# Optimization experiments

Hardware: AMD Instinct MI355X
Metric: run time of the kernel (lower is better)

## Reference

```python
import jax, jax.numpy as jnp
import numpy as np

CODEBOOK_SIZE = 1024
CODEWORD_SIZE = 256
BETA = 0.1
N_INIT = 1  # embedding ~ U(-1/n, 1/n)


def setup_inputs() -> dict:
    key = jax.random.key(0)
    kx, ke = jax.random.split(key)
    x = jax.random.normal(kx, (16, 4096, CODEWORD_SIZE), dtype=jnp.float32)
    embedding = jax.random.uniform(
        ke, (CODEBOOK_SIZE, CODEWORD_SIZE), dtype=jnp.float32,
        minval=-1.0 / N_INIT, maxval=1.0 / N_INIT)
    return {"x": x, "embedding": embedding}


def reference(x, embedding):
    dist = (jnp.sum(x * x, axis=2, keepdims=True)
            + jnp.sum(embedding * embedding, axis=1)
            - 2.0 * jnp.einsum('btd,kd->btk', x, embedding))
    indexes = jnp.argmin(dist, axis=2)              # [B,T] int
    values = jnp.take(embedding, indexes, axis=0)   # gather == one_hot @ embedding
    sg = jax.lax.stop_gradient
    loss1 = jnp.mean((sg(x) - values) ** 2)         # codebook loss
    loss2 = jnp.mean((x - sg(values)) ** 2)         # commitment loss
    loss = loss1 + BETA * loss2
    values_st = x + sg(values - x)                  # straight-through
    return values_st, indexes, loss
```

## Files before the change

kernel.cpp:

```cpp
#include <hip/hip_runtime.h>
#include <stdint.h>


#define BT    65536
#define D     256
#define KCB   1024
#define BM    256
#define BN    128
#define NTT   (KCB/BN)
#define BK    32

typedef float    f32x4 __attribute__((ext_vector_type(4)));
typedef _Float16 f16x8 __attribute__((ext_vector_type(8)));

#define GLOAD_LDS16(g, l) \
  __builtin_amdgcn_global_load_lds((const __attribute__((address_space(1))) void*)(g), \
                                   (__attribute__((address_space(3))) void*)(l), 16, 0, 0)

__global__ __launch_bounds__(256) void split_e_kernel(const float* __restrict__ E,
                                                      _Float16* __restrict__ Eh,
                                                      _Float16* __restrict__ El,
                                                      float* __restrict__ enorm,
                                                      float* __restrict__ out_loss) {
    if (blockIdx.x == 0 && threadIdx.x == 0) *out_loss = 0.f;
    const int r = blockIdx.x * 8 + (threadIdx.x >> 5);
    const size_t i0 = (size_t)r * D + (threadIdx.x & 31) * 8;
    float4 v0 = *(const float4*)(E + i0);
    float4 v1 = *(const float4*)(E + i0 + 4);
    float v[8] = {v0.x, v0.y, v0.z, v0.w, v1.x, v1.y, v1.z, v1.w};
    f16x8 h, l;
    float s = 0.f;
    #pragma unroll
    for (int j = 0; j < 8; ++j) {
        _Float16 hh = (_Float16)v[j];
        h[j] = hh;
        l[j] = (_Float16)(v[j] - (float)hh);
        s += v[j] * v[j];
    }
    *(f16x8*)(Eh + i0) = h;
    *(f16x8*)(El + i0) = l;
    #pragma unroll
    for (int off = 1; off < 32; off <<= 1) s += __shfl_xor(s, off, 64);
    if ((threadIdx.x & 31) == 0) enorm[r] = s;
}

__global__ __launch_bounds__(512, 2) void vq_mfma_kernel(
    const float* __restrict__ X,
    const _Float16* __restrict__ Eh, const _Float16* __restrict__ El,
    const float* __restrict__ enorm, const float* __restrict__ E,
    float* __restrict__ out_vals, float* __restrict__ out_idx,
    float* __restrict__ out_loss) {
    __shared__ __align__(16) float    Xs[64 * D];
    __shared__ __align__(16) _Float16 Bsh[2][BN * BK];
    __shared__ __align__(16) _Float16 Bsl[2][BN * BK];
    __shared__ float s_en[KCB];
    __shared__ float s_bd[BM];
    __shared__ int   s_bi[BM];
    __shared__ float s_red[8];

    const int tid  = threadIdx.x;
    const int w    = tid >> 6;
    const int lane = tid & 63;
    const int quad = lane >> 4;
    const int l16  = lane & 15;
    const int sxa  = l16 & 7;
    const int row0 = blockIdx.x * BM;

    const int sb_row = lane >> 2;
    const int sb_off = ((((lane & 3) - (lane >> 3)) & 3) << 3);
    const int kob = ((quad + ((l16 >> 1) & 3)) & 3) << 3;

    auto STAGE_B = [&](int buf, int col0, int kb) {
        const int gr = col0 + w * 16 + sb_row;
        const size_t gb = (size_t)gr * D + kb + sb_off;
        GLOAD_LDS16(Eh + gb, &Bsh[buf][w * 512]);
        GLOAD_LDS16(El + gb, &Bsl[buf][w * 512]);
    };

    s_en[tid]       = enorm[tid];
    s_en[tid + 512] = enorm[tid + 512];

    STAGE_B(0, 0, 0);

    f16x8 pah[2][8], pal[2][8];
    float xs = 0.f;
    for (int p = 0; p < 4; ++p) {
        #pragma unroll
        for (int rr = 0; rr < 8; ++rr) {
            const int sr = w * 8 + rr;
            const int gr = row0 + p * 64 + sr;
            GLOAD_LDS16(X + (size_t)gr * D + ((lane ^ rr) << 2), &Xs[sr * D]);
        }
        asm volatile("s_waitcnt vmcnt(0) lgkmcnt(0)" ::: "memory");
        __builtin_amdgcn_s_barrier();
        if ((w >> 1) == p) {
            const int srb = (w & 1) * 32;
            #pragma unroll
            for (int i = 0; i < 2; ++i) {
                const float* rp = &Xs[(srb + i * 16 + l16) * D];
                #pragma unroll
                for (int kc = 0; kc < 8; ++kc) {
                    const int c0 = kc * 8 + quad * 2;
                    const f32x4 v0 = *(const f32x4*)(rp + (((c0)     ^ sxa) << 2));
                    const f32x4 v1 = *(const f32x4*)(rp + (((c0 | 1) ^ sxa) << 2));
                    const float f[8] = {v0.x, v0.y, v0.z, v0.w, v1.x, v1.y, v1.z, v1.w};
                    #pragma unroll
                    for (int e = 0; e < 8; ++e) {
                        const _Float16 hh = (_Float16)f[e];
                        pah[i][kc][e] = hh;
                        pal[i][kc][e] = (_Float16)(f[e] - (float)hh);
                        xs += f[e] * f[e];
                    }
                }
            }
        }
        __builtin_amdgcn_s_barrier();
    }

    float rb_d[2][4];
    int   rb_i[2][4];
    #pragma unroll
    for (int i = 0; i < 2; ++i)
        #pragma unroll
        for (int r = 0; r < 4; ++r) { rb_d[i][r] = 3.4e38f; rb_i[i][r] = 0; }
    f32x4 acc[2][8];

    for (int nt = 0; nt < NTT; ++nt) {
        const int col0 = nt * BN;
        #pragma unroll
        for (int kc = 0; kc < 8; ++kc) {
            const int cur = kc & 1;
            if (kc < 7) {
                STAGE_B(cur ^ 1, col0, (kc + 1) * BK);
                asm volatile("s_waitcnt vmcnt(2)" ::: "memory");
            } else if (nt < NTT - 1) {
                STAGE_B(cur ^ 1, col0 + BN, 0);
                asm volatile("s_waitcnt vmcnt(2)" ::: "memory");
            } else {
                asm volatile("s_waitcnt vmcnt(0)" ::: "memory");
            }
            __builtin_amdgcn_s_barrier();

            if (kc == 0) {
                #pragma unroll
                for (int i = 0; i < 2; ++i)
                    #pragma unroll
                    for (int j = 0; j < 8; ++j) acc[i][j] = (f32x4)0.0f;
            }

            const _Float16* Bh = Bsh[cur];
            const _Float16* Bl = Bsl[cur];

            __builtin_amdgcn_s_setprio(1);
            #pragma unroll
            for (int j = 0; j < 8; ++j) {
                const int n = (j * 16 + l16) * BK + kob;
                const f16x8 bh = *(const f16x8*)&Bh[n];
                const f16x8 bl = *(const f16x8*)&Bl[n];
                #pragma unroll
                for (int i = 0; i < 2; ++i) {
                    acc[i][j] = __builtin_amdgcn_mfma_f32_16x16x32_f16(pah[i][kc], bh, acc[i][j], 0, 0, 0);
                    acc[i][j] = __builtin_amdgcn_mfma_f32_16x16x32_f16(pal[i][kc], bh, acc[i][j], 0, 0, 0);
                    acc[i][j] = __builtin_amdgcn_mfma_f32_16x16x32_f16(pah[i][kc], bl, acc[i][j], 0, 0, 0);
                }
            }
            __builtin_amdgcn_s_setprio(0);

            if (kc == 7) {
                #pragma unroll
                for (int j = 0; j < 8; ++j) {
                    const int c = col0 + j * 16 + l16;
                    const float en = s_en[c];
                    #pragma unroll
                    for (int i = 0; i < 2; ++i)
                        #pragma unroll
                        for (int r = 0; r < 4; ++r) {
                            const float sd = en - 2.0f * acc[i][j][r];
                            if (sd < rb_d[i][r]) { rb_d[i][r] = sd; rb_i[i][r] = c; }
                        }
                }
            }
            __builtin_amdgcn_s_barrier();
        }
    }

    #pragma unroll
    for (int off = 1; off < 16; off <<= 1) {
        #pragma unroll
        for (int i = 0; i < 2; ++i)
            #pragma unroll
            for (int r = 0; r < 4; ++r) {
                const float od = __shfl_xor(rb_d[i][r], off, 64);
                const int   oi = __shfl_xor(rb_i[i][r], off, 64);
                if (od < rb_d[i][r] || (od == rb_d[i][r] && oi < rb_i[i][r])) {
                    rb_d[i][r] = od; rb_i[i][r] = oi;
                }
            }
    }
    if (l16 == 0) {
        #pragma unroll
        for (int i = 0; i < 2; ++i)
            #pragma unroll
            for (int r = 0; r < 4; ++r) {
                const int m = w * 32 + i * 16 + quad * 4 + r;
                s_bd[m] = rb_d[i][r]; s_bi[m] = rb_i[i][r];
            }
    }
    __syncthreads();

    float part = xs;
    if (tid < BM) {
        out_idx[row0 + tid] = (float)s_bi[tid];
        part += s_bd[tid];
    }

    const int col = tid & 255;
    const int sub = tid >> 8;
    #pragma unroll 4
    for (int it = 0; it < BM / 2; ++it) {
        const int r  = it * 2 + sub;
        const int bi = s_bi[r];
        out_vals[(size_t)(row0 + r) * D + col] = E[(size_t)bi * D + col];
    }

    #pragma unroll
    for (int off = 1; off < 64; off <<= 1) part += __shfl_xor(part, off, 64);
    if (lane == 0) s_red[w] = part;
    __syncthreads();
    if (tid == 0) {
        float tot = 0.f;
        #pragma unroll
        for (int i = 0; i < 8; ++i) tot += s_red[i];
        atomicAdd(out_loss, tot * (1.1f / 16777216.f));
    }
}

extern "C" void kernel_launch(void* const* d_in, const int* in_sizes, int n_in,
                              void* d_out, int out_size, void* d_ws, size_t ws_size,
                              hipStream_t stream) {
    const float* X = (const float*)d_in[0];
    const float* E = (const float*)d_in[1];
    float* out      = (float*)d_out;
    float* out_vals = out;
    float* out_idx  = out + (size_t)BT * D;
    float* out_loss = out + (size_t)BT * D + BT;

    char* ws = (char*)d_ws;
    _Float16* Eh    = (_Float16*)ws;
    _Float16* El    = Eh + (size_t)KCB * D;
    float*    enorm = (float*)(El + (size_t)KCB * D);
    (void)ws_size; (void)n_in; (void)in_sizes; (void)out_size;

    split_e_kernel<<<KCB / 8, 256, 0, stream>>>(E, Eh, El, enorm, out_loss);
    vq_mfma_kernel<<<BT / BM, 512, 0, stream>>>(X, Eh, El, enorm, E,
                                                out_vals, out_idx, out_loss);
}
```

Baseline: 193.8 us.

## Stage two K-chunks per barrier and alias X staging with codebook buffers

Each pipeline step now loads and consumes two BK chunks of the fp16 hi/lo codebook, which halves the number of barrier pairs per column tile. The X staging buffer is unioned with the double-buffered codebook tiles to keep shared memory in check. Pipeline depth stays at one step ahead, with a larger vmcnt window. The risk is longer exposed load latency per step and reuse of LDS that the X staging pass also writes; the first codebook stage is moved until after X staging finishes.

```diff
diff --git a/kernel.cpp b/kernel.cpp
--- a/kernel.cpp
+++ b/kernel.cpp
@@ -7,7 +7,6 @@
 #define KCB   1024
 #define BM    256
 #define BN    128
-#define NTT   (KCB/BN)
 #define BK    32
 
 typedef float    f32x4 __attribute__((ext_vector_type(4)));
@@ -50,13 +49,14 @@
     const float* __restrict__ enorm, const float* __restrict__ E,
     float* __restrict__ out_vals, float* __restrict__ out_idx,
     float* __restrict__ out_loss) {
-    __shared__ __align__(16) float    Xs[64 * D];
-    __shared__ __align__(16) _Float16 Bsh[2][BN * BK];
-    __shared__ __align__(16) _Float16 Bsl[2][BN * BK];
+    __shared__ __align__(16) char Bmem[8 * BN * BK * 2];
     __shared__ float s_en[KCB];
     __shared__ float s_bd[BM];
     __shared__ int   s_bi[BM];
     __shared__ float s_red[8];
+
+    float*    const Xs = (float*)Bmem;
+    _Float16* const BB = (_Float16*)Bmem;
 
     const int tid  = threadIdx.x;
     const int w    = tid >> 6;
@@ -70,17 +70,20 @@
     const int sb_off = ((((lane & 3) - (lane >> 3)) & 3) << 3);
     const int kob = ((quad + ((l16 >> 1) & 3)) & 3) << 3;
 
-    auto STAGE_B = [&](int buf, int col0, int kb) {
-        const int gr = col0 + w * 16 + sb_row;
-        const size_t gb = (size_t)gr * D + kb + sb_off;
-        GLOAD_LDS16(Eh + gb, &Bsh[buf][w * 512]);
-        GLOAD_LDS16(El + gb, &Bsl[buf][w * 512]);
+    auto STAGE_PH = [&](int buf, int step) {
+        const int col0 = (step >> 2) * BN;
+        const int kb0  = (step & 3) * (2 * BK);
+        #pragma unroll
+        for (int h = 0; h < 2; ++h) {
+            const int gr = col0 + w * 16 + sb_row;
+            const size_t gb = (size_t)gr * D + kb0 + h * BK + sb_off;
+            GLOAD_LDS16(Eh + gb, BB + (buf * 4 + h * 2 + 0) * (BN * BK) + w * 512);
+            GLOAD_LDS16(El + gb, BB + (buf * 4 + h * 2 + 1) * (BN * BK) + w * 512);
+        }
     };
 
     s_en[tid]       = enorm[tid];
     s_en[tid + 512] = enorm[tid + 512];
-
-    STAGE_B(0, 0, 0);
 
     f16x8 pah[2][8], pal[2][8];
     float xs = 0.f;
@@ -125,48 +128,49 @@
         for (int r = 0; r < 4; ++r) { rb_d[i][r] = 3.4e38f; rb_i[i][r] = 0; }
     f32x4 acc[2][8];
 
-    for (int nt = 0; nt < NTT; ++nt) {
+    STAGE_PH(0, 0);
+    for (int nt = 0; nt < 8; ++nt) {
         const int col0 = nt * BN;
         #pragma unroll
-        for (int kc = 0; kc < 8; ++kc) {
-            const int cur = kc & 1;
-            if (kc < 7) {
-                STAGE_B(cur ^ 1, col0, (kc + 1) * BK);
-                asm volatile("s_waitcnt vmcnt(2)" ::: "memory");
-            } else if (nt < NTT - 1) {
-                STAGE_B(cur ^ 1, col0 + BN, 0);
-                asm volatile("s_waitcnt vmcnt(2)" ::: "memory");
+        for (int q = 0; q < 4; ++q) {
+            const int cur = q & 1;
+            if (nt == 7 && q == 3) {
+                asm volatile("s_waitcnt vmcnt(0)" ::: "memory");
             } else {
-                asm volatile("s_waitcnt vmcnt(0)" ::: "memory");
+                STAGE_PH(cur ^ 1, nt * 4 + q + 1);
+                asm volatile("s_waitcnt vmcnt(4)" ::: "memory");
             }
             __builtin_amdgcn_s_barrier();
 
-            if (kc == 0) {
+            if (q == 0) {
                 #pragma unroll
                 for (int i = 0; i < 2; ++i)
                     #pragma unroll
                     for (int j = 0; j < 8; ++j) acc[i][j] = (f32x4)0.0f;
             }
 
-            const _Float16* Bh = Bsh[cur];
-            const _Float16* Bl = Bsl[cur];
-
-            __builtin_amdgcn_s_setprio(1);
-            #pragma unroll
-            for (int j = 0; j < 8; ++j) {
-                const int n = (j * 16 + l16) * BK + kob;
-                const f16x8 bh = *(const f16x8*)&Bh[n];
-                const f16x8 bl = *(const f16x8*)&Bl[n];
-                #pragma unroll
-                for (int i = 0; i < 2; ++i) {
-                    acc[i][j] = __builtin_amdgcn_mfma_f32_16x16x32_f16(pah[i][kc], bh, acc[i][j], 0, 0, 0);
-                    acc[i][j] = __builtin_amdgcn_mfma_f32_16x16x32_f16(pal[i][kc], bh, acc[i][j], 0, 0, 0);
-                    acc[i][j] = __builtin_amdgcn_mfma_f32_16x16x32_f16(pah[i][kc], bl, acc[i][j], 0, 0, 0);
-                }
-            }
-            __builtin_amdgcn_s_setprio(0);
-
-            if (kc == 7) {
+            #pragma unroll
+            for (int sub = 0; sub < 2; ++sub) {
+                const int kc = q * 2 + sub;
+                const _Float16* Bh = BB + (cur * 4 + sub * 2 + 0) * (BN * BK);
+                const _Float16* Bl = BB + (cur * 4 + sub * 2 + 1) * (BN * BK);
+                __builtin_amdgcn_s_setprio(1);
+                #pragma unroll
+                for (int j = 0; j < 8; ++j) {
+                    const int n = (j * 16 + l16) * BK + kob;
+                    const f16x8 bh = *(const f16x8*)&Bh[n];
+                    const f16x8 bl = *(const f16x8*)&Bl[n];
+                    #pragma unroll
+                    for (int i = 0; i < 2; ++i) {
+                        acc[i][j] = __builtin_amdgcn_mfma_f32_16x16x32_f16(pah[i][kc], bh, acc[i][j], 0, 0, 0);
+                        acc[i][j] = __builtin_amdgcn_mfma_f32_16x16x32_f16(pal[i][kc], bh, acc[i][j], 0, 0, 0);
+                        acc[i][j] = __builtin_amdgcn_mfma_f32_16x16x32_f16(pah[i][kc], bl, acc[i][j], 0, 0, 0);
+                    }
+                }
+                __builtin_amdgcn_s_setprio(0);
+            }
+
+            if (q == 3) {
                 #pragma unroll
                 for (int j = 0; j < 8; ++j) {
                     const int c = col0 + j * 16 + l16;
```

Measured after the change: 189.9 us. 1.02x faster.
